# Optimization experiments

Measured on AMD Instinct MI355X. Metric: run time of the kernel, lower is better.

## Reference

```python
import jax, jax.numpy as jnp
import numpy as np

B, CIN, H, W = 32, 512, 16, 16
COUT, HEADS, SPARSITY = 2048, 8, 7
D = COUT // HEADS  # 256, must equal H*W
N = H * W


def conv1x1(x, w, b):
    # x: [B,C,H,W], w: [O,C], b: [O]
    return jnp.einsum('bchw,oc->bohw', x, w) + b[None, :, None, None]


def setup_inputs() -> dict:
    key = jax.random.key(0)
    ks = jax.random.split(key, 11)
    def lin(k, o, c):
        bound = 1.0 / np.sqrt(c)
        kw, kb = jax.random.split(k)
        return (jax.random.uniform(kw, (o, c), jnp.float32, -bound, bound),
                jax.random.uniform(kb, (o,), jnp.float32, -bound, bound))
    Wq, bq = lin(ks[0], COUT, CIN)
    Wk, bk = lin(ks[1], COUT, CIN)
    Wv, bv = lin(ks[2], COUT, CIN)
    Wo, bo = lin(ks[3], COUT, COUT)
    # kaiming_uniform_ on [COUT, COUT]
    gain = np.sqrt(2.0) / np.sqrt(5.0)  # default a=sqrt(5)
    bound = gain * np.sqrt(3.0 / COUT)
    coeff = jax.random.uniform(ks[4], (COUT, COUT), jnp.float32, -bound, bound)
    scale = jnp.array([np.sqrt(D)], jnp.float32)
    x = jax.random.normal(ks[5], (B, CIN, H, W), jnp.float32)
    return {"x": x, "Wq": Wq, "bq": bq, "Wk": Wk, "bk": bk, "Wv": Wv,
            "bv": bv, "Wo": Wo, "bo": bo, "coeff": coeff, "scale": scale}


def reference(x, Wq, bq, Wk, bk, Wv, bv, Wo, bo, coeff, scale):
    # enforce_sparsity: keep top-`SPARSITY` |coeff| per row, zero the rest
    _, idx = jax.lax.top_k(jnp.abs(coeff), SPARSITY)  # [COUT, SPARSITY]
    mask = jnp.zeros(coeff.shape, bool).at[jnp.arange(COUT)[:, None], idx].set(True)
    coeff_s = jnp.where(mask, coeff, 0.0)

    q = conv1x1(x, Wq, bq).reshape(B, HEADS, D, N)
    k = conv1x1(x, Wk, bk).reshape(B, HEADS, D, N)
    v = conv1x1(x, Wv, bv).reshape(B, HEADS, D, N)

    attn = jnp.einsum('bhdn,bhdm->bhnm', q, k) / scale[0]  # [B,h,N,N]
    sparse_attn = jnp.einsum('bhnm,mp->bhnp', attn, coeff_s[:D, :D])
    sparse_attn = jax.nn.softmax(sparse_attn, axis=-1)
    out = jnp.einsum('bhnm,bhmd->bhnd', sparse_attn, v.transpose(0, 1, 3, 2))
    out = out.transpose(0, 1, 3, 2).reshape(B, COUT, H, W)
    return conv1x1(out, Wo, bo)
```

## Files before the change

kernel.cpp:

```cpp
#include <hip/hip_runtime.h>

typedef unsigned short ushort;
typedef __attribute__((ext_vector_type(8))) short short8;
typedef __attribute__((ext_vector_type(8))) unsigned short ushort8;
typedef __attribute__((ext_vector_type(4))) unsigned short ushort4v;
typedef __attribute__((ext_vector_type(4))) float fx4;

#define MAXNNZ (256*7)

__device__ __forceinline__ ushort f2bf(float f) {
    union { float f; unsigned u; } v; v.f = f;
    unsigned r = v.u + 0x7fffu + ((v.u >> 16) & 1u);
    return (ushort)(r >> 16);
}

__device__ __forceinline__ float bf2f(ushort b) {
    union { unsigned u; float f; } v; v.u = ((unsigned)b) << 16;
    return v.f;
}

__device__ __forceinline__ void gload_lds16(const ushort* g, ushort* l) {
    __builtin_amdgcn_global_load_lds(
        (const __attribute__((address_space(1))) unsigned int*)g,
        (__attribute__((address_space(3))) unsigned int*)l, 16, 0, 0);
}

__global__ __launch_bounds__(256)
void topk_kernel(const float* __restrict__ coeff,
                 int* __restrict__ coo_cnt, int* __restrict__ coo_m,
                 int* __restrict__ coo_p, float* __restrict__ coo_v)
{
    int row = blockIdx.x;
    int tid = threadIdx.x;
    const float* crow = coeff + (long)row * 2048;
    float av[8];
#pragma unroll
    for (int i = 0; i < 8; ++i) av[i] = fabsf(crow[tid + 256 * i]);
    __shared__ unsigned long long red[256];
    for (int t = 0; t < 7; ++t) {
        float mx = -1.f; int mi = 0;
#pragma unroll
        for (int i = 0; i < 8; ++i) if (av[i] > mx) { mx = av[i]; mi = i; }
        unsigned col = (unsigned)(tid + 256 * mi);
        unsigned long long pk = ((unsigned long long)__float_as_uint(mx) << 32)
                              | (unsigned long long)(2048u - col);
        red[tid] = pk; __syncthreads();
        for (int s = 128; s > 0; s >>= 1) {
            if (tid < s) { if (red[tid + s] > red[tid]) red[tid] = red[tid + s]; }
            __syncthreads();
        }
        unsigned long long w = red[0];
        __syncthreads();
        unsigned wcol = 2048u - (unsigned)(w & 0xffffffffu);
        if ((wcol & 255u) == (unsigned)tid) av[wcol >> 8] = -1.f;
        if (tid == 0 && wcol < 256u) {
            int pos = atomicAdd(coo_cnt, 1);
            coo_m[pos] = row; coo_p[pos] = (int)wcol; coo_v[pos] = crow[wcol];
        }
    }
}

__global__ __launch_bounds__(256)
void csc_kernel(const int* __restrict__ coo_cnt, const int* __restrict__ coo_m,
                const int* __restrict__ coo_p, const float* __restrict__ coo_v,
                int* __restrict__ csc_ptr, int* __restrict__ csc_m, float* __restrict__ csc_v)
{
    __shared__ int cnt[256];
    __shared__ int off[257];
    __shared__ int cur[256];
    int tid = threadIdx.x;
    cnt[tid] = 0;
    __syncthreads();
    int n = *coo_cnt; if (n > MAXNNZ) n = MAXNNZ;
    for (int e = tid; e < n; e += 256) atomicAdd(&cnt[coo_p[e]], 1);
    __syncthreads();
    if (tid == 0) {
        int s = 0;
        for (int p = 0; p < 256; ++p) { off[p] = s; s += cnt[p]; }
        off[256] = s;
    }
    __syncthreads();
    csc_ptr[tid] = off[tid];
    if (tid == 0) csc_ptr[256] = off[256];
    cur[tid] = off[tid];
    __syncthreads();
    for (int e = tid; e < n; e += 256) {
        int p = coo_p[e];
        int pos = atomicAdd(&cur[p], 1);
        csc_m[pos] = coo_m[e];
        csc_v[pos] = coo_v[e];
    }
}

__global__ void cvt4_kernel(const float* a0, ushort* d0, int n0,
                            const float* a1, ushort* d1, int n1,
                            const float* a2, ushort* d2, int n2,
                            const float* a3, ushort* d3, int n3)
{
    const float* s; ushort* d; int n;
    switch (blockIdx.y) {
        case 0: s = a0; d = d0; n = n0; break;
        case 1: s = a1; d = d1; n = n1; break;
        case 2: s = a2; d = d2; n = n2; break;
        default: s = a3; d = d3; n = n3; break;
    }
    int nv = n >> 2;
    for (int i = blockIdx.x * blockDim.x + threadIdx.x; i < nv; i += gridDim.x * blockDim.x) {
        fx4 v = ((const fx4*)s)[i];
        ushort4v o;
        o[0] = f2bf(v[0]); o[1] = f2bf(v[1]); o[2] = f2bf(v[2]); o[3] = f2bf(v[3]);
        ((ushort4v*)d)[i] = o;
    }
}

__global__ __launch_bounds__(256)
void transpose_f32_bf16(const float* __restrict__ in, ushort* __restrict__ out, int R, int C)
{
    int z = blockIdx.z;
    const float* ib = in + (long)z * R * C;
    ushort* ob = out + (long)z * R * C;
    __shared__ ushort tile[64][72];
    int r0 = blockIdx.x * 64, c0 = blockIdx.y * 64;
    int tid = threadIdx.x;
    int rl = tid >> 2, sg = tid & 3;
#pragma unroll
    for (int h = 0; h < 4; ++h) {
        fx4 v = *(const fx4*)(ib + (long)(r0 + rl) * C + c0 + h * 16 + sg * 4);
#pragma unroll
        for (int i = 0; i < 4; ++i) tile[h * 16 + sg * 4 + i][rl] = f2bf(v[i]);
    }
    __syncthreads();
    int cl = rl;
#pragma unroll
    for (int h = 0; h < 2; ++h) {
        ushort8 vv = *(const ushort8*)(&tile[cl][h * 32 + sg * 8]);
        *(ushort8*)(ob + (long)(c0 + cl) * R + r0 + h * 32 + sg * 8) = vv;
    }
}

__global__ __launch_bounds__(256)
void kcomb_kernel(const ushort* __restrict__ kbT, ushort* __restrict__ ktc,
                  const int* __restrict__ csc_ptr, const int* __restrict__ csc_m,
                  const float* __restrict__ csc_v)
{
    int z = blockIdx.y;
    int tid = threadIdx.x;
    int p = blockIdx.x * 64 + (tid >> 2);
    int d0 = (tid & 3) * 64;
    const ushort* src = kbT + (long)z * 65536;
    float acc[64];
#pragma unroll
    for (int i = 0; i < 64; ++i) acc[i] = 0.f;
    int e0 = csc_ptr[p], e1 = csc_ptr[p + 1];
    for (int e = e0; e < e1; ++e) {
        const ushort* row = src + csc_m[e] * 256 + d0;
        float c = csc_v[e];
#pragma unroll
        for (int u = 0; u < 8; ++u) {
            ushort8 v = *(const ushort8*)(row + u * 8);
#pragma unroll
            for (int t = 0; t < 8; ++t) acc[u * 8 + t] += bf2f(v[t]) * c;
        }
    }
    ushort* dst = ktc + (long)z * 65536 + (long)p * 256 + d0;
#pragma unroll
    for (int u = 0; u < 8; ++u) {
        ushort8 o;
#pragma unroll
        for (int t = 0; t < 8; ++t) o[t] = f2bf(acc[u * 8 + t]);
        *(ushort8*)(dst + u * 8) = o;
    }
}

__global__ __launch_bounds__(256, 2)
void attn_kernel(const ushort* __restrict__ Q, const ushort* __restrict__ Kt,
                 const ushort* __restrict__ V, ushort* __restrict__ O,
                 const float* __restrict__ scale_src)
{
    __shared__ __align__(16) ushort PQ[32768];
    __shared__ float rmax[4][128];
    __shared__ float rsum[4][128];

    int bid = blockIdx.x;
    int hf = bid >> 8, z = bid & 255;
    int b = z >> 3, h = z & 7;
    const ushort* Qz = Q + (long)z * 65536 + (long)hf * 32768;
    const ushort* Kz = Kt + (long)z * 65536;
    const ushort* Vz = V + (long)b * 524288 + (long)h * 65536;
    ushort* Ob = O + (long)b * 524288 + (long)h * 256 + (long)hf * 128 * 2048;

    int tid = threadIdx.x;
    int wave = tid >> 6, lane = tid & 63;
    int l16 = lane & 15, quad = lane >> 4;
    int key = l16 & 7;

    {
        int rb = wave * 2 + (lane >> 5);
        const ushort* qsrc = Qz + (long)rb * 256 + (((lane & 31) ^ (rb & 7)) * 8);
        ushort* qdst = PQ + wave * 512;
#pragma unroll
        for (int g = 0; g < 16; ++g)
            gload_lds16(qsrc + g * 2048, qdst + g * 2048);
    }

    const ushort* kfp = Kz + (long)(wave * 64 + l16) * 256 + quad * 8;
    const ushort* vfp = Vz + (long)(wave * 64 + l16) * 256 + quad * 8;

    fx4 acc[8][4];
#pragma unroll
    for (int i = 0; i < 8; ++i)
#pragma unroll
        for (int j = 0; j < 4; ++j) acc[i][j] = (fx4){0.f, 0.f, 0.f, 0.f};

    short8 bfn[4];
#pragma unroll
    for (int j = 0; j < 4; ++j) bfn[j] = *(const short8*)(kfp + j * 4096);

    __syncthreads();

    float sc = 1.0f / scale_src[0];

#pragma unroll
    for (int kd = 0; kd < 8; ++kd) {
        short8 bf[4];
#pragma unroll
        for (int j = 0; j < 4; ++j) bf[j] = bfn[j];
        if (kd < 7) {
#pragma unroll
            for (int j = 0; j < 4; ++j)
                bfn[j] = *(const short8*)(kfp + j * 4096 + (kd + 1) * 32);
        }
        short8 af[8];
#pragma unroll
        for (int i = 0; i < 8; ++i)
            af[i] = *(const short8*)(PQ + (i * 16 + l16) * 256 + (((kd * 4 + quad) ^ key) * 8));
        __builtin_amdgcn_s_setprio(1);
#pragma unroll
        for (int i = 0; i < 8; ++i)
#pragma unroll
            for (int j = 0; j < 4; ++j)
                acc[i][j] = __builtin_amdgcn_mfma_f32_16x16x32_bf16(af[i], bf[j], acc[i][j], 0, 0, 0);
        __builtin_amdgcn_s_setprio(0);
    }

#pragma unroll
    for (int i = 0; i < 8; ++i)
#pragma unroll
        for (int j = 0; j < 4; ++j)
#pragma unroll
            for (int r = 0; r < 4; ++r) acc[i][j][r] *= sc;

    float lm[8][4];
#pragma unroll
    for (int i = 0; i < 8; ++i)
#pragma unroll
        for (int r = 0; r < 4; ++r) {
            float m = -1e30f;
#pragma unroll
            for (int j = 0; j < 4; ++j) m = fmaxf(m, acc[i][j][r]);
            lm[i][r] = m;
        }
#pragma unroll
    for (int d = 1; d < 16; d <<= 1)
#pragma unroll
        for (int i = 0; i < 8; ++i)
#pragma unroll
            for (int r = 0; r < 4; ++r) lm[i][r] = fmaxf(lm[i][r], __shfl_xor(lm[i][r], d, 16));
    if (l16 == 0) {
#pragma unroll
        for (int i = 0; i < 8; ++i)
#pragma unroll
            for (int r = 0; r < 4; ++r)
                rmax[wave][i * 16 + quad * 4 + r] = lm[i][r];
    }
    __syncthreads();

    float ls[8][4];
#pragma unroll
    for (int i = 0; i < 8; ++i)
#pragma unroll
        for (int r = 0; r < 4; ++r) {
            int row = i * 16 + quad * 4 + r;
            float M = fmaxf(fmaxf(rmax[0][row], rmax[1][row]),
                            fmaxf(rmax[2][row], rmax[3][row]));
            float s = 0.f;
#pragma unroll
            for (int j = 0; j < 4; ++j) {
                float e = __expf(acc[i][j][r] - M);
                acc[i][j][r] = e;
                s += e;
            }
            ls[i][r] = s;
        }
#pragma unroll
    for (int d = 1; d < 16; d <<= 1)
#pragma unroll
        for (int i = 0; i < 8; ++i)
#pragma unroll
            for (int r = 0; r < 4; ++r) ls[i][r] += __shfl_xor(ls[i][r], d, 16);
    if (l16 == 0) {
#pragma unroll
        for (int i = 0; i < 8; ++i)
#pragma unroll
            for (int r = 0; r < 4; ++r)
                rsum[wave][i * 16 + quad * 4 + r] = ls[i][r];
    }
    __syncthreads();

    short8 vfn[4];
#pragma unroll
    for (int j = 0; j < 4; ++j) vfn[j] = *(const short8*)(vfp + j * 4096);

#pragma unroll
    for (int i = 0; i < 8; ++i)
#pragma unroll
        for (int r = 0; r < 4; ++r) {
            int row = i * 16 + quad * 4 + r;
            float inv = 1.0f / (rsum[0][row] + rsum[1][row] + rsum[2][row] + rsum[3][row]);
            int k2 = row & 7;
#pragma unroll
            for (int j = 0; j < 4; ++j) {
                int p = wave * 64 + j * 16 + l16;
                PQ[row * 256 + ((((p >> 3) ^ k2) << 3) | (p & 7))] = f2bf(acc[i][j][r] * inv);
            }
        }
    __syncthreads();

    fx4 acc2[8][4];
#pragma unroll
    for (int i = 0; i < 8; ++i)
#pragma unroll
        for (int j = 0; j < 4; ++j) acc2[i][j] = (fx4){0.f, 0.f, 0.f, 0.f};

#pragma unroll
    for (int kp = 0; kp < 8; ++kp) {
        short8 vf[4];
#pragma unroll
        for (int j = 0; j < 4; ++j) vf[j] = vfn[j];
        if (kp < 7) {
#pragma unroll
            for (int j = 0; j < 4; ++j)
                vfn[j] = *(const short8*)(vfp + j * 4096 + (kp + 1) * 32);
        }
        short8 pa[8];
#pragma unroll
        for (int i = 0; i < 8; ++i)
            pa[i] = *(const short8*)(PQ + (i * 16 + l16) * 256 + (((kp * 4 + quad) ^ key) * 8));
        __builtin_amdgcn_s_setprio(1);
#pragma unroll
        for (int i = 0; i < 8; ++i)
#pragma unroll
            for (int j = 0; j < 4; ++j)
                acc2[i][j] = __builtin_amdgcn_mfma_f32_16x16x32_bf16(pa[i], vf[j], acc2[i][j], 0, 0, 0);
        __builtin_amdgcn_s_setprio(0);
    }

    __syncthreads();
#pragma unroll
    for (int i = 0; i < 8; ++i)
#pragma unroll
        for (int j = 0; j < 4; ++j) {
            int rowb = i * 16 + quad * 4;
            int col = wave * 64 + j * 16 + l16;
#pragma unroll
            for (int rr = 0; rr < 4; ++rr) {
                int row = rowb + rr;
                PQ[row * 256 + ((((col >> 3) ^ (row & 7)) << 3) | (col & 7))]
                    = f2bf(acc2[i][j][rr]);
            }
        }
    __syncthreads();
#pragma unroll
    for (int pass = 0; pass < 16; ++pass) {
        int row = pass * 8 + (tid >> 5), ch = tid & 31;
        ushort8 vv = *(const ushort8*)(PQ + row * 256 + ((ch ^ (row & 7)) << 3));
        *(ushort8*)(Ob + (long)row * 2048 + ch * 8) = vv;
    }
}

template<int MODE>
__global__ __launch_bounds__(512, 2)
void gemm256(const ushort* __restrict__ A, const ushort* __restrict__ B,
             void* __restrict__ C,
             const float* __restrict__ bias0, const float* __restrict__ bias1,
             const float* __restrict__ bias2,
             int MT, int K)
{
    __shared__ __align__(16) ushort lds[4][2][8192];

    int nwg = gridDim.x;
    int bid = blockIdx.x;
    int cpx = nwg >> 3;
    int swz = (bid & 7) * cpx + (bid >> 3);
    int mt = swz % MT, nt = swz / MT;
    int m0 = mt << 8, n0 = nt << 8;

    int tid = threadIdx.x;
    int wave = tid >> 6, lane = tid & 63;
    int wr = wave >> 2, wc = wave & 3;
    int l16 = lane & 15, quad = lane >> 4;

    int lc = (((lane & 3) ^ ((lane >> 3) & 3))) * 8;
    const ushort* gA0 = A + (long long)(m0 + wave * 16 + (lane >> 2)) * K + lc;
    const ushort* gA1 = gA0 + (long long)128 * K;
    const ushort* gB0 = B + (long long)(n0 + wave * 16 + (lane >> 2)) * K + lc;
    const ushort* gB1 = gB0 + (long long)128 * K;
    int ldso = wave * 512;

    int rsw = ((l16 >> 1) & 3) * 8;
    int aoff = (wr * 128 + l16) * 32 + ((quad * 8) ^ rsw);
    int boff = (wc * 64 + l16) * 32 + ((quad * 8) ^ rsw);

    fx4 acc[8][4];
#pragma unroll
    for (int i = 0; i < 8; ++i)
#pragma unroll
        for (int j = 0; j < 4; ++j) acc[i][j] = (fx4){0.f, 0.f, 0.f, 0.f};

    auto stageA = [&](int b, int kc) {
        gload_lds16(gA0 + kc, &lds[b][0][ldso]);
        gload_lds16(gA1 + kc, &lds[b][0][4096 + ldso]);
    };
    auto stageB = [&](int b, int kc) {
        gload_lds16(gB0 + kc, &lds[b][1][ldso]);
        gload_lds16(gB1 + kc, &lds[b][1][4096 + ldso]);
    };

    short8 af[4], bf[4];
    auto readA = [&](int b, int half) {
        const ushort* p = &lds[b][0][aoff + half * 2048];
#pragma unroll
        for (int i = 0; i < 4; ++i) af[i] = *(const short8*)(p + i * 512);
    };
    auto readB = [&](int b) {
        const ushort* p = &lds[b][1][boff];
#pragma unroll
        for (int j = 0; j < 4; ++j) bf[j] = *(const short8*)(p + j * 512);
    };
    auto mma = [&](int half) {
        __builtin_amdgcn_s_setprio(1);
#pragma unroll
        for (int i = 0; i < 4; ++i)
#pragma unroll
            for (int j = 0; j < 4; ++j)
                acc[half * 4 + i][j] =
                    __builtin_amdgcn_mfma_f32_16x16x32_bf16(af[i], bf[j], acc[half * 4 + i][j], 0, 0, 0);
        __builtin_amdgcn_s_setprio(0);
    };

    int NT = K >> 5;
    stageA(0, 0);  stageB(0, 0);
    stageA(1, 32); stageB(1, 32);
    stageA(2, 64); stageB(2, 64);
    asm volatile("s_waitcnt vmcnt(8)" ::: "memory");
    __builtin_amdgcn_s_barrier();

    for (int t = 0; t < NT; ++t) {
        int b = t & 3;
        readA(b, 0); readB(b);
        if (t + 3 < NT) stageA((t + 3) & 3, (t + 3) << 5);
        __builtin_amdgcn_s_barrier();
        asm volatile("s_waitcnt lgkmcnt(0)" ::: "memory");
        __builtin_amdgcn_sched_barrier(0);
        mma(0);
        __builtin_amdgcn_s_barrier();
        readA(b, 1);
        if (t + 3 < NT) {
            stageB((t + 3) & 3, (t + 3) << 5);
            asm volatile("s_waitcnt vmcnt(8)" ::: "memory");
        } else if (t + 2 < NT) {
            asm volatile("s_waitcnt vmcnt(4)" ::: "memory");
        } else if (t + 1 < NT) {
            asm volatile("s_waitcnt vmcnt(0)" ::: "memory");
        }
        __builtin_amdgcn_s_barrier();
        asm volatile("s_waitcnt lgkmcnt(0)" ::: "memory");
        __builtin_amdgcn_sched_barrier(0);
        mma(1);
        __builtin_amdgcn_s_barrier();
    }

    if (MODE == 5) {
        float* Cf = (float*)C + (long long)nt * 524288;
#pragma unroll
        for (int i = 0; i < 8; ++i) {
            int m = m0 + wr * 128 + i * 16 + quad * 4;
#pragma unroll
            for (int j = 0; j < 4; ++j) {
                int n = wc * 64 + j * 16 + l16;
                float* dst = Cf + (long long)m * 256 + n;
#pragma unroll
                for (int r = 0; r < 4; ++r)
                    dst[(long)r * 256] = acc[i][j][r] + bias0[m + r];
            }
        }
        return;
    }

    if (MODE == 4) {
        int sec = m0 >> 11;
        int ms0 = m0 & 2047;
        ushort* ct = &lds[0][0][0];
        if (sec < 2) {
            const float* bs = (sec == 0) ? bias0 : bias1;
            ushort* base = (ushort*)C + (long long)sec * 16777216
                         + (long long)nt * 524288 + (long long)(ms0 >> 8) * 65536;
#pragma unroll
            for (int hh = 0; hh < 2; ++hh) {
                if ((wc >> 1) == hh) {
#pragma unroll
                    for (int i = 0; i < 8; ++i)
#pragma unroll
                        for (int j = 0; j < 4; ++j) {
                            int nl = (wc & 1) * 64 + j * 16 + l16;
                            int ml = wr * 128 + i * 16 + quad * 4;
                            ushort4v pk;
#pragma unroll
                            for (int r = 0; r < 4; ++r)
                                pk[r] = f2bf(acc[i][j][r] + bs[ms0 + ml + r]);
                            *(ushort4v*)(ct + nl * 264 + ml) = pk;
                        }
                }
                __syncthreads();
                int row = tid & 127, c0 = (tid >> 7) * 64;
                ushort* dst = base + (long long)(hh * 128 + row) * 256 + c0;
                const ushort* src = ct + row * 264 + c0;
#pragma unroll
                for (int u = 0; u < 8; ++u)
                    *(ushort8*)(dst + u * 8) = *(const ushort8*)(src + u * 8);
                __syncthreads();
            }
        } else {
            ushort* base = (ushort*)C + 33554432LL + (long long)nt * 524288
                         + (long long)ms0 * 256;
#pragma unroll
            for (int hh = 0; hh < 2; ++hh) {
                if (wr == hh) {
#pragma unroll
                    for (int i = 0; i < 8; ++i)
#pragma unroll
                        for (int j = 0; j < 4; ++j) {
                            int nl = wc * 64 + j * 16 + l16;
                            int ml = i * 16 + quad * 4;
#pragma unroll
                            for (int r = 0; r < 4; ++r)
                                ct[(ml + r) * 264 + nl] =
                                    f2bf(acc[i][j][r] + bias2[ms0 + hh * 128 + ml + r]);
                        }
                }
                __syncthreads();
                int row = tid & 127, c0 = (tid >> 7) * 64;
                ushort* dst = base + (long long)(hh * 128 + row) * 256 + c0;
                const ushort* src = ct + row * 264 + c0;
#pragma unroll
                for (int u = 0; u < 8; ++u)
                    *(ushort8*)(dst + u * 8) = *(const ushort8*)(src + u * 8);
                __syncthreads();
            }
        }
        return;
    }
}

extern "C" void kernel_launch(void* const* d_in, const int* in_sizes, int n_in,
                              void* d_out, int out_size, void* d_ws, size_t ws_size,
                              hipStream_t stream)
{
    const float* x     = (const float*)d_in[0];
    const float* Wq    = (const float*)d_in[1];
    const float* bq    = (const float*)d_in[2];
    const float* Wk    = (const float*)d_in[3];
    const float* bk    = (const float*)d_in[4];
    const float* Wv    = (const float*)d_in[5];
    const float* bv    = (const float*)d_in[6];
    const float* Wo    = (const float*)d_in[7];
    const float* bo    = (const float*)d_in[8];
    const float* coeff = (const float*)d_in[9];
    const float* scale = (const float*)d_in[10];
    float* out = (float*)d_out;

    size_t o = 0;
    char* w = (char*)d_ws;
    auto take = [&](size_t bytes) -> void* {
        void* p = w + o; o += (bytes + 255) & ~(size_t)255; return p;
    };
    int*    coo_cnt = (int*)take(4);
    int*    coo_m   = (int*)take(MAXNNZ * 4);
    int*    coo_p   = (int*)take(MAXNNZ * 4);
    float*  coo_v   = (float*)take(MAXNNZ * 4);
    int*    csc_ptr = (int*)take(257 * 4);
    int*    csc_m   = (int*)take(MAXNNZ * 4);
    float*  csc_v   = (float*)take(MAXNNZ * 4);
    ushort* wqkv = (ushort*)take(6144L * 512 * 2);
    ushort* wob  = (ushort*)take(2048L * 2048 * 2);
    ushort* xT   = (ushort*)take(32L * 256 * 512 * 2);
    ushort* qkv  = (ushort*)take(3 * 16777216L * 2);
    ushort* qbT = qkv;
    ushort* kbT = qkv + 16777216L;
    ushort* vb  = qkv + 33554432L;
    ushort* ktc = (ushort*)take(16777216L * 2);
    ushort* obT  = kbT;
    (void)in_sizes; (void)n_in; (void)out_size; (void)ws_size;

    hipMemsetAsync(coo_cnt, 0, 4, stream);
    topk_kernel<<<256, 256, 0, stream>>>(coeff, coo_cnt, coo_m, coo_p, coo_v);
    csc_kernel<<<1, 256, 0, stream>>>(coo_cnt, coo_m, coo_p, coo_v, csc_ptr, csc_m, csc_v);

    cvt4_kernel<<<dim3(1024, 4, 1), 256, 0, stream>>>(
        Wq, wqkv, 2048 * 512, Wk, wqkv + 2048L * 512, 2048 * 512,
        Wv, wqkv + 4096L * 512, 2048 * 512, Wo, wob, 2048 * 2048);
    transpose_f32_bf16<<<dim3(8, 4, 32), 256, 0, stream>>>(x, xT, 512, 256);

    gemm256<4><<<dim3(768, 1, 1), dim3(512, 1, 1), 0, stream>>>(
        wqkv, xT, qkv, bq, bk, bv, 24, 512);

    kcomb_kernel<<<dim3(4, 256), 256, 0, stream>>>(kbT, ktc, csc_ptr, csc_m, csc_v);

    attn_kernel<<<512, 256, 0, stream>>>(qbT, ktc, vb, obT, scale);

    gemm256<5><<<dim3(256, 1, 1), dim3(512, 1, 1), 0, stream>>>(
        wob, obT, out, bo, nullptr, nullptr, 8, 2048);
}
```

Measured before the change: 381.1 us.

## Apply sparse coefficient mixing to input x before K projection instead of after

Since the K projection is linear, the sparse coefficient combine is moved from the projected K tensor onto the smaller transposed input x. The K section of the QKV GEMM then reads the combined input, and its bias is scaled by per-column coefficient sums computed in the CSC kernel. This removes the large combine pass over K. It also adds an XCD-aware tile mapping for the QKV GEMM. The trade-off is that the bf16 rounding order changes, since x is combined and rounded before the projection.

```diff
diff --git a/kernel.cpp b/kernel.cpp
--- a/kernel.cpp
+++ b/kernel.cpp
@@ -63,7 +63,8 @@
 __global__ __launch_bounds__(256)
 void csc_kernel(const int* __restrict__ coo_cnt, const int* __restrict__ coo_m,
                 const int* __restrict__ coo_p, const float* __restrict__ coo_v,
-                int* __restrict__ csc_ptr, int* __restrict__ csc_m, float* __restrict__ csc_v)
+                int* __restrict__ csc_ptr, int* __restrict__ csc_m,
+                float* __restrict__ csc_v, float* __restrict__ csum)
 {
     __shared__ int cnt[256];
     __shared__ int off[257];
@@ -89,6 +90,13 @@
         int pos = atomicAdd(&cur[p], 1);
         csc_m[pos] = coo_m[e];
         csc_v[pos] = coo_v[e];
+    }
+    __syncthreads();
+    {
+        float s = 0.f;
+        int e0 = off[tid], e1 = off[tid] + cnt[tid];
+        for (int e = e0; e < e1; ++e) s += csc_v[e];
+        csum[tid] = s;
     }
 }
 
@@ -139,21 +147,21 @@
 }
 
 __global__ __launch_bounds__(256)
-void kcomb_kernel(const ushort* __restrict__ kbT, ushort* __restrict__ ktc,
+void xcomb_kernel(const ushort* __restrict__ xT, ushort* __restrict__ xc,
                   const int* __restrict__ csc_ptr, const int* __restrict__ csc_m,
                   const float* __restrict__ csc_v)
 {
-    int z = blockIdx.y;
+    int b = blockIdx.y;
     int tid = threadIdx.x;
-    int p = blockIdx.x * 64 + (tid >> 2);
-    int d0 = (tid & 3) * 64;
-    const ushort* src = kbT + (long)z * 65536;
+    int p = blockIdx.x * 32 + (tid >> 3);
+    int c0 = (tid & 7) * 64;
+    const ushort* src = xT + (long)b * 131072;
     float acc[64];
 #pragma unroll
     for (int i = 0; i < 64; ++i) acc[i] = 0.f;
     int e0 = csc_ptr[p], e1 = csc_ptr[p + 1];
     for (int e = e0; e < e1; ++e) {
-        const ushort* row = src + csc_m[e] * 256 + d0;
+        const ushort* row = src + csc_m[e] * 512 + c0;
         float c = csc_v[e];
 #pragma unroll
         for (int u = 0; u < 8; ++u) {
@@ -162,7 +170,7 @@
             for (int t = 0; t < 8; ++t) acc[u * 8 + t] += bf2f(v[t]) * c;
         }
     }
-    ushort* dst = ktc + (long)z * 65536 + (long)p * 256 + d0;
+    ushort* dst = xc + (long)b * 131072 + (long)p * 512 + c0;
 #pragma unroll
     for (int u = 0; u < 8; ++u) {
         ushort8 o;
@@ -381,29 +389,40 @@
 template<int MODE>
 __global__ __launch_bounds__(512, 2)
 void gemm256(const ushort* __restrict__ A, const ushort* __restrict__ B,
-             void* __restrict__ C,
+             const ushort* __restrict__ B2, void* __restrict__ C,
+             ushort* __restrict__ Kout,
              const float* __restrict__ bias0, const float* __restrict__ bias1,
-             const float* __restrict__ bias2,
+             const float* __restrict__ bias2, const float* __restrict__ csum,
              int MT, int K)
 {
     __shared__ __align__(16) ushort lds[4][2][8192];
 
     int nwg = gridDim.x;
     int bid = blockIdx.x;
-    int cpx = nwg >> 3;
-    int swz = (bid & 7) * cpx + (bid >> 3);
-    int mt = swz % MT, nt = swz / MT;
+    int mt, nt;
+    if (MODE == 4) {
+        int xcd = bid & 7, idx = bid >> 3;
+        mt = (xcd & 1) * 12 + idx % 12;
+        nt = (xcd >> 1) * 8 + idx / 12;
+    } else {
+        int cpx = nwg >> 3;
+        int swz = (bid & 7) * cpx + (bid >> 3);
+        mt = swz % MT; nt = swz / MT;
+    }
     int m0 = mt << 8, n0 = nt << 8;
+    int sec = m0 >> 11;
 
     int tid = threadIdx.x;
     int wave = tid >> 6, lane = tid & 63;
     int wr = wave >> 2, wc = wave & 3;
     int l16 = lane & 15, quad = lane >> 4;
 
+    const ushort* Bb = (MODE == 4 && sec == 1) ? B2 : B;
+
     int lc = (((lane & 3) ^ ((lane >> 3) & 3))) * 8;
     const ushort* gA0 = A + (long long)(m0 + wave * 16 + (lane >> 2)) * K + lc;
     const ushort* gA1 = gA0 + (long long)128 * K;
-    const ushort* gB0 = B + (long long)(n0 + wave * 16 + (lane >> 2)) * K + lc;
+    const ushort* gB0 = Bb + (long long)(n0 + wave * 16 + (lane >> 2)) * K + lc;
     const ushort* gB1 = gB0 + (long long)128 * K;
     int ldso = wave * 512;
 
@@ -498,12 +517,11 @@
     }
 
     if (MODE == 4) {
-        int sec = m0 >> 11;
         int ms0 = m0 & 2047;
         ushort* ct = &lds[0][0][0];
         if (sec < 2) {
             const float* bs = (sec == 0) ? bias0 : bias1;
-            ushort* base = (ushort*)C + (long long)sec * 16777216
+            ushort* base = ((sec == 0) ? (ushort*)C : Kout)
                          + (long long)nt * 524288 + (long long)(ms0 >> 8) * 65536;
 #pragma unroll
             for (int hh = 0; hh < 2; ++hh) {
@@ -514,10 +532,11 @@
                         for (int j = 0; j < 4; ++j) {
                             int nl = (wc & 1) * 64 + j * 16 + l16;
                             int ml = wr * 128 + i * 16 + quad * 4;
+                            float csf = (sec == 1) ? csum[hh * 128 + nl] : 1.0f;
                             ushort4v pk;
 #pragma unroll
                             for (int r = 0; r < 4; ++r)
-                                pk[r] = f2bf(acc[i][j][r] + bs[ms0 + ml + r]);
+                                pk[r] = f2bf(acc[i][j][r] + bs[ms0 + ml + r] * csf);
                             *(ushort4v*)(ct + nl * 264 + ml) = pk;
                         }
                 }
@@ -591,33 +610,36 @@
     int*    csc_ptr = (int*)take(257 * 4);
     int*    csc_m   = (int*)take(MAXNNZ * 4);
     float*  csc_v   = (float*)take(MAXNNZ * 4);
+    float*  csum    = (float*)take(256 * 4);
     ushort* wqkv = (ushort*)take(6144L * 512 * 2);
     ushort* wob  = (ushort*)take(2048L * 2048 * 2);
     ushort* xT   = (ushort*)take(32L * 256 * 512 * 2);
     ushort* qkv  = (ushort*)take(3 * 16777216L * 2);
     ushort* qbT = qkv;
-    ushort* kbT = qkv + 16777216L;
+    ushort* mid = qkv + 16777216L;
     ushort* vb  = qkv + 33554432L;
     ushort* ktc = (ushort*)take(16777216L * 2);
-    ushort* obT  = kbT;
+    ushort* xc  = mid;
+    ushort* obT = mid;
     (void)in_sizes; (void)n_in; (void)out_size; (void)ws_size;
 
     hipMemsetAsync(coo_cnt, 0, 4, stream);
     topk_kernel<<<256, 256, 0, stream>>>(coeff, coo_cnt, coo_m, coo_p, coo_v);
-    csc_kernel<<<1, 256, 0, stream>>>(coo_cnt, coo_m, coo_p, coo_v, csc_ptr, csc_m, csc_v);
+    csc_kernel<<<1, 256, 0, stream>>>(coo_cnt, coo_m, coo_p, coo_v,
+                                      csc_ptr, csc_m, csc_v, csum);
 
     cvt4_kernel<<<dim3(1024, 4, 1), 256, 0, stream>>>(
         Wq, wqkv, 2048 * 512, Wk, wqkv + 2048L * 512, 2048 * 512,
         Wv, wqkv + 4096L * 512, 2048 * 512, Wo, wob, 2048 * 2048);
     transpose_f32_bf16<<<dim3(8, 4, 32), 256, 0, stream>>>(x, xT, 512, 256);
 
+    xcomb_kernel<<<dim3(8, 32), 256, 0, stream>>>(xT, xc, csc_ptr, csc_m, csc_v);
+
     gemm256<4><<<dim3(768, 1, 1), dim3(512, 1, 1), 0, stream>>>(
-        wqkv, xT, qkv, bq, bk, bv, 24, 512);
-
-    kcomb_kernel<<<dim3(4, 256), 256, 0, stream>>>(kbT, ktc, csc_ptr, csc_m, csc_v);
+        wqkv, xT, xc, qkv, ktc, bq, bk, bv, csum, 24, 512);
 
     attn_kernel<<<512, 256, 0, stream>>>(qbT, ktc, vb, obT, scale);
 
     gemm256<5><<<dim3(256, 1, 1), dim3(512, 1, 1), 0, stream>>>(
-        wob, obT, out, bo, nullptr, nullptr, 8, 2048);
-}
+        wob, obT, nullptr, out, nullptr, bo, nullptr, nullptr, nullptr, 8, 2048);
+}
```

Measured after the change: 364.2 us. -4.4%, faster.
